# Kernel tuning notes

Hardware: AMD Instinct MI355X
Metric: run time of the kernel (lower is better)

## Reference

```python
import jax, jax.numpy as jnp
import numpy as np
from jax import lax

L_LAYERS = 8
HID = 300


def _reverse_padded(x, lengths):
    # x: [T, B, D]; reverse each sequence within its valid length, keep padding zero.
    T = x.shape[0]
    t = jnp.arange(T)[:, None]                      # [T,1]
    rev = lengths[None, :] - 1 - t                  # [T,B]
    valid = (rev >= 0)
    idx = jnp.clip(rev, 0, T - 1)
    g = jnp.take_along_axis(x, idx[:, :, None].astype(jnp.int32), axis=0)
    return g * valid[:, :, None].astype(x.dtype)


def _run_layer(x, W_ih, W_hh, b, lengths, reverse):
    # x: [T,B,D] time-major. W_ih: [D,6H], W_hh: [H,5H], b: [5H]
    T, B, _ = x.shape
    H = W_hh.shape[0]
    if reverse:
        x = _reverse_padded(x, lengths)
    pi = jnp.einsum('tbd,dg->tbg', x, W_ih)         # [T,B,6H] input projections
    mask = (jnp.arange(T)[:, None] < lengths[None, :])[:, :, None]  # [T,B,1] bool

    def step(carry, xt):
        h, c = carry
        pi_t, m = xt
        ps = h @ W_hh + b                            # [B,5H]
        z = pi_t[:, :5 * H] + ps                     # fused pre-activations
        i = jax.nn.sigmoid(z[:, 0 * H:1 * H])
        f = jax.nn.sigmoid(z[:, 1 * H:2 * H])
        g = jnp.tanh(z[:, 2 * H:3 * H])
        o = jax.nn.sigmoid(z[:, 3 * H:4 * H])
        r = jax.nn.sigmoid(z[:, 4 * H:5 * H])        # highway gate
        c_new = i * g + f * c
        lstm_out = o * jnp.tanh(c_new)
        h_new = r * lstm_out + (1.0 - r) * pi_t[:, 5 * H:]  # highway connection
        c = jnp.where(m, c_new, c)
        h = jnp.where(m, h_new, h)
        return (h, c), h_new * m.astype(h_new.dtype)

    init = (jnp.zeros((B, H), x.dtype), jnp.zeros((B, H), x.dtype))
    (_, _), ys = lax.scan(step, init, (pi, mask))
    if reverse:
        ys = _reverse_padded(ys, lengths)
    return ys


def setup_inputs() -> dict:
    key = jax.random.key(0)
    ks = jax.random.split(key, 6)
    B, T, D = 64, 256, 200
    inputs = jax.random.normal(ks[0], (B, T, D), dtype=jnp.float32)
    lengths = jnp.sort(jax.random.randint(ks[1], (B,), 1, T + 1))[::-1].astype(jnp.int32)
    s = 0.08
    W_ih0 = jax.random.normal(ks[2], (D, 6 * HID), dtype=jnp.float32) * s
    W_ih_rest = jax.random.normal(ks[3], (L_LAYERS - 1, HID, 6 * HID), dtype=jnp.float32) * s
    W_hh = jax.random.normal(ks[4], (L_LAYERS, HID, 5 * HID), dtype=jnp.float32) * s
    b_hh = jnp.zeros((L_LAYERS, 5 * HID), dtype=jnp.float32)
    b_hh = b_hh.at[:, HID:2 * HID].set(1.0)  # forget-gate bias init to 1
    return {"inputs": inputs, "lengths": lengths, "W_ih0": W_ih0,
            "W_ih_rest": W_ih_rest, "W_hh": W_hh, "b_hh": b_hh}


def reference(inputs, lengths, W_ih0, W_ih_rest, W_hh, b_hh):
    # inputs: [B,T,D] batch-first -> time-major [T,B,D]
    x = jnp.transpose(inputs, (1, 0, 2))
    per_layer = []
    for layer in range(L_LAYERS):
        Wih = W_ih0 if layer == 0 else W_ih_rest[layer - 1]
        x = _run_layer(x, Wih, W_hh[layer], b_hh[layer], lengths, reverse=(layer % 2 == 1))
        per_layer.append(x)
    hidden = jnp.stack(per_layer)                    # [L,T,B,H] (matches hy[:,1:])
    output = jnp.transpose(x, (1, 0, 2))             # [B,T,H], zero past lengths
    return output, hidden
```

## Files before the change

kernel.cpp:

```cpp
#include <hip/hip_runtime.h>
#include <hip/hip_bf16.h>

#define B_ 64
#define T_ 256
#define D_ 200
#define H_ 300
#define L_ 8
#define M_ 16384
#define NG 1800
#define NZ 1500
#define KP 320
#define NBP 1920

typedef __attribute__((ext_vector_type(8))) short bf16x8;
typedef __attribute__((ext_vector_type(4))) float f32x4;
typedef __attribute__((ext_vector_type(4))) unsigned u32x4;
typedef unsigned long long ull;

__device__ __forceinline__ unsigned short f2bf(float f) {
  union { float f; unsigned u; } v; v.f = f;
  unsigned r = v.u + 0x7fffu + ((v.u >> 16) & 1u);
  return (unsigned short)(r >> 16);
}

__device__ __forceinline__ float sigf(float x) { return 1.f / (1.f + __expf(-x)); }
__device__ __forceinline__ float tanhf_(float x) {
  x = fminf(15.f, fmaxf(-15.f, x));
  float e = __expf(2.f * x);
  return (e - 1.f) / (e + 1.f);
}

#define BARRIER() asm volatile("s_waitcnt lgkmcnt(0)\n\ts_barrier" ::: "memory")

__device__ __forceinline__ u32x4 ld128_nt(const ull* p) {
  u32x4 v;
  asm volatile("global_load_dwordx4 %0, %1, off nt\n\ts_waitcnt vmcnt(0)"
               : "=v"(v) : "v"(p) : "memory");
  return v;
}
__device__ __forceinline__ u32x4 ld128_sys(const ull* p) {
  u32x4 v;
  asm volatile("global_load_dwordx4 %0, %1, off sc0 sc1\n\ts_waitcnt vmcnt(0)"
               : "=v"(v) : "v"(p) : "memory");
  return v;
}
__device__ __forceinline__ void st64_plain(ull* p, ull v) {
  asm volatile("global_store_dwordx2 %0, %1, off" :: "v"(p), "v"(v) : "memory");
}
__device__ __forceinline__ void st64_sys(ull* p, ull v) {
  asm volatile("global_store_dwordx2 %0, %1, off sc0 sc1" :: "v"(p), "v"(v) : "memory");
}

__device__ __forceinline__ void gl_lds16(const unsigned short* g, unsigned short* l) {
  __builtin_amdgcn_global_load_lds(
      (const __attribute__((address_space(1))) void*)g,
      (__attribute__((address_space(3))) void*)l, 16, 0, 0);
}

__global__ void k_transpose_w(const float* __restrict__ W0, const float* __restrict__ Wr,
                              unsigned short* __restrict__ WbT) {
  __shared__ unsigned short t_lds[64][65];
  const int n0 = blockIdx.x * 64;
  const int k0 = blockIdx.y * 64;
  const int l = blockIdx.z;
  const int Kl = (l == 0) ? D_ : H_;
  const float* W = (l == 0) ? W0 : (Wr + (size_t)(l - 1) * H_ * NG);
  unsigned short* out = WbT + (size_t)l * NBP * KP;
  const int tx = threadIdx.x & 63;
  const int ty = threadIdx.x >> 6;
  #pragma unroll
  for (int i = 0; i < 16; i++) {
    int k = k0 + ty * 16 + i;
    int n = n0 + tx;
    float v = (k < Kl && n < NG) ? W[(size_t)k * NG + n] : 0.f;
    t_lds[ty * 16 + i][tx] = f2bf(v);
  }
  __syncthreads();
  #pragma unroll
  for (int i = 0; i < 16; i++) {
    int n = n0 + ty * 16 + i;
    if (n < NG) out[(size_t)n * KP + k0 + tx] = t_lds[tx][ty * 16 + i];
  }
}

__global__ void k_transpose_in(const float* __restrict__ inp, unsigned short* __restrict__ xb) {
  int i = blockIdx.x * blockDim.x + threadIdx.x;
  if (i >= T_ * B_ * D_) return;
  int d = i % D_;
  int r = i / D_;
  int b = r % B_;
  int t = r / B_;
  xb[(size_t)r * KP + d] = f2bf(inp[((size_t)b * T_ + t) * D_ + d]);
}

__global__ void k_out(const float* __restrict__ hid7, float* __restrict__ outp) {
  int i = blockIdx.x * blockDim.x + threadIdx.x;
  if (i >= B_ * T_ * H_) return;
  int j = i % H_;
  int r = i / H_;
  int t = r % T_;
  int b = r / T_;
  outp[i] = hid7[((size_t)t * B_ + b) * H_ + j];
}

__global__ __launch_bounds__(256) void k_gemm(const unsigned short* __restrict__ A,
                                              const unsigned short* __restrict__ Bt,
                                              float* __restrict__ C, int nk) {
  __shared__ unsigned short As[128 * 32];
  __shared__ unsigned short Bs[128 * 32];
  const int bm = blockIdx.x, bn = blockIdx.y;
  const int tid = threadIdx.x;
  const int lane = tid & 63, wid = tid >> 6;
  const int wm = wid & 1, wn = wid >> 1;
  const int l16 = lane & 15, quad = lane >> 4;
  const int srow = lane >> 2;
  const int sswz = ((lane & 3) ^ (srow & 3)) << 3;
  const int sA = ((quad ^ (l16 & 3)) << 3);
  const size_t arow0 = (size_t)bm * 128;
  const size_t brow0 = (size_t)bn * 128;
  f32x4 acc[4][4] = {};
  for (int kc = 0; kc < nk; kc++) {
    const int k0 = kc << 5;
    #pragma unroll
    for (int r = 0; r < 2; r++) {
      const int rbase = r * 64 + wid * 16;
      gl_lds16(A  + (arow0 + rbase + srow) * KP + k0 + sswz, &As[rbase * 32]);
      gl_lds16(Bt + (brow0 + rbase + srow) * KP + k0 + sswz, &Bs[rbase * 32]);
    }
    asm volatile("s_waitcnt vmcnt(0)" ::: "memory");
    __syncthreads();
    bf16x8 af[4], bfr[4];
    #pragma unroll
    for (int i = 0; i < 4; i++) {
      af[i]  = *(const bf16x8*)&As[(wm * 64 + i * 16 + l16) * 32 + sA];
      bfr[i] = *(const bf16x8*)&Bs[(wn * 64 + i * 16 + l16) * 32 + sA];
    }
    #pragma unroll
    for (int mi = 0; mi < 4; mi++)
      #pragma unroll
      for (int ni = 0; ni < 4; ni++)
        acc[mi][ni] = __builtin_amdgcn_mfma_f32_16x16x32_bf16(af[mi], bfr[ni], acc[mi][ni], 0, 0, 0);
    __syncthreads();
  }
  const int row0 = bm * 128 + wm * 64 + quad * 4;
  const int col0 = bn * 128 + wn * 64 + l16;
  #pragma unroll
  for (int mi = 0; mi < 4; mi++) {
    #pragma unroll
    for (int ni = 0; ni < 4; ni++) {
      int col = col0 + ni * 16;
      if (col < NG) {
        #pragma unroll
        for (int i = 0; i < 4; i++)
          C[(size_t)(row0 + mi * 16 + i) * NG + col] = acc[mi][ni][i];
      }
    }
  }
}

__global__ __launch_bounds__(512, 2) void k_recur(
    const float* __restrict__ pi, const float* __restrict__ Whh,
    const float* __restrict__ bias, const int* __restrict__ lens,
    float* __restrict__ hid, unsigned short* __restrict__ xb,
    ull* __restrict__ h_words, int rev, int tagbase)
{
  __shared__ __align__(16) unsigned short h_lds[16 * 328];
  __shared__ __align__(16) float z_lds[128 * 4];
  __shared__ float bias_s[128];
  __shared__ int len_s[4];

  const int tid = threadIdx.x;
  const int bid = blockIdx.x;
  const int g = bid & 15;
  const int cb = bid >> 4;

  const int lane = tid & 63;
  const int wid = tid >> 6;
  const int l16 = lane & 15;
  const int quad = lane >> 4;

  const int rp = tid / 25;
  const int gj = tid - rp * 25;
  const int j2 = cb * 25 + gj;

  bf16x8 wfrag[10];
  {
    int n = wid * 16 + l16;
    bool vn = n < 125;
    int colw = vn ? ((n / 25) * 300 + cb * 25 + (n % 25)) : 0;
    #pragma unroll
    for (int c = 0; c < 10; c++) {
      bf16x8 f;
      #pragma unroll
      for (int j = 0; j < 8; j++) {
        int k = c * 32 + quad * 8 + j;
        float v = (vn && k < 300) ? Whh[(size_t)k * NZ + colw] : 0.f;
        f[j] = (short)f2bf(v);
      }
      wfrag[c] = f;
    }
  }
  if (tid < 4) len_s[tid] = lens[g * 4 + tid];
  if (tid < 125) bias_s[tid] = bias[(tid / 25) * 300 + cb * 25 + (tid % 25)];
  for (int i = tid; i < 16 * 328; i += 512) h_lds[i] = 0;
  __syncthreads();

  int S = len_s[0];
  S = len_s[1] > S ? len_s[1] : S;
  S = len_s[2] > S ? len_s[2] : S;
  S = len_s[3] > S ? len_s[3] : S;

  ull* hwf = h_words + (size_t)g * 1200;
  ull* hws = h_words + 16 * 1200 + (size_t)g * 1200;
  const int brbase = g * 4;
  float cA = 0.f, cB = 0.f;

  float pA0 = 0.f, pA1 = 0.f, pA2 = 0.f, pA3 = 0.f, pA4 = 0.f, pA6 = 0.f;
  float pB0 = 0.f, pB1 = 0.f, pB2 = 0.f, pB3 = 0.f, pB4 = 0.f, pB6 = 0.f;
#define PI_PREF(ss) do {                                                          \
    int lrA_ = len_s[2 * rp], lrB_ = len_s[2 * rp + 1];                           \
    pA0 = pA1 = pA2 = pA3 = pA4 = pA6 = 0.f;                                      \
    pB0 = pB1 = pB2 = pB3 = pB4 = pB6 = 0.f;                                      \
    if ((ss) < lrA_) {                                                            \
      int t_ = rev ? (lrA_ - 1 - (ss)) : (ss);                                    \
      const float* pr_ = pi + ((size_t)t_ * B_ + (brbase + 2 * rp)) * NG;         \
      pA0 = pr_[j2]; pA1 = pr_[300 + j2]; pA2 = pr_[600 + j2];                    \
      pA3 = pr_[900 + j2]; pA4 = pr_[1200 + j2]; pA6 = pr_[NZ + j2];              \
    }                                                                             \
    if ((ss) < lrB_) {                                                            \
      int t_ = rev ? (lrB_ - 1 - (ss)) : (ss);                                    \
      const float* pr_ = pi + ((size_t)t_ * B_ + (brbase + 2 * rp + 1)) * NG;     \
      pB0 = pr_[j2]; pB1 = pr_[300 + j2]; pB2 = pr_[600 + j2];                    \
      pB3 = pr_[900 + j2]; pB4 = pr_[1200 + j2]; pB6 = pr_[NZ + j2];              \
    }                                                                             \
  } while (0)
  if (tid < 50) PI_PREF(0);

  for (int s = 0; s < S; s++) {
    if (s > 0 && tid >= 64 && tid < 364) {
      const unsigned tg = (unsigned)(tagbase + s);
      const size_t par = (size_t)(s & 1) * 600;
      const int pt = tid - 64;
      const ull* pf = hwf + par + 2 * pt;
      const ull* ps = hws + par + 2 * pt;
      u32x4 v;
      int miss = 0;
      for (;;) {
        v = ld128_nt(pf);
        if ((v.y == tg) && (v.w == tg)) break;
        if ((++miss & 31) == 0) {
          v = ld128_sys(ps);
          if ((v.y == tg) && (v.w == tg)) break;
          __builtin_amdgcn_s_sleep(1);
        }
      }
      int w0 = pt << 1;
      int r2 = (w0 >= 300) ? 1 : 0;
      int k = w0 - r2 * 300;
      h_lds[(2 * r2) * 328 + k]     = (unsigned short)(v.x >> 16);
      h_lds[(2 * r2 + 1) * 328 + k] = (unsigned short)(v.x & 0xffffu);
      int w1 = w0 + 1;
      int r2b = (w1 >= 300) ? 1 : 0;
      int kb = w1 - r2b * 300;
      h_lds[(2 * r2b) * 328 + kb]     = (unsigned short)(v.z >> 16);
      h_lds[(2 * r2b + 1) * 328 + kb] = (unsigned short)(v.z & 0xffffu);
    }
    BARRIER();

    f32x4 acc = {0, 0, 0, 0};
    if (s > 0) {
      f32x4 acc2 = {0, 0, 0, 0};
      const unsigned short* abase = &h_lds[l16 * 328 + quad * 8];
      #pragma unroll
      for (int c = 0; c < 10; c += 2) {
        bf16x8 a0 = *(const bf16x8*)(abase + c * 32);
        bf16x8 a1 = *(const bf16x8*)(abase + c * 32 + 32);
        acc  = __builtin_amdgcn_mfma_f32_16x16x32_bf16(a0, wfrag[c],     acc,  0, 0, 0);
        acc2 = __builtin_amdgcn_mfma_f32_16x16x32_bf16(a1, wfrag[c + 1], acc2, 0, 0, 0);
      }
      acc += acc2;
    }
    if (quad == 0) {
      int n = wid * 16 + l16;
      *(f32x4*)&z_lds[n * 4] = acc;
    }
    BARRIER();

    if (tid < 50) {
      const float bb0 = bias_s[gj],      bb1 = bias_s[25 + gj], bb2 = bias_s[50 + gj];
      const float bb3 = bias_s[75 + gj], bb4 = bias_s[100 + gj];
      const float2 z0 = *(const float2*)&z_lds[(gj      ) * 4 + 2 * rp];
      const float2 z1 = *(const float2*)&z_lds[(25 + gj ) * 4 + 2 * rp];
      const float2 z2 = *(const float2*)&z_lds[(50 + gj ) * 4 + 2 * rp];
      const float2 z3 = *(const float2*)&z_lds[(75 + gj ) * 4 + 2 * rp];
      const float2 z4 = *(const float2*)&z_lds[(100 + gj) * 4 + 2 * rp];
      float iA = sigf(z0.x + pA0 + bb0);
      float fA = sigf(z1.x + pA1 + bb1);
      float gA = tanhf_(z2.x + pA2 + bb2);
      float oA = sigf(z3.x + pA3 + bb3);
      float rA = sigf(z4.x + pA4 + bb4);
      float cnA = iA * gA + fA * cA; cA = cnA;
      float hA = rA * (oA * tanhf_(cnA)) + (1.f - rA) * pA6;
      float iB = sigf(z0.y + pB0 + bb0);
      float fB = sigf(z1.y + pB1 + bb1);
      float gB = tanhf_(z2.y + pB2 + bb2);
      float oB = sigf(z3.y + pB3 + bb3);
      float rB = sigf(z4.y + pB4 + bb4);
      float cnB = iB * gB + fB * cB; cB = cnB;
      float hB = rB * (oB * tanhf_(cnB)) + (1.f - rB) * pB6;

      unsigned short hbA = f2bf(hA), hbB = f2bf(hB);
      ull word = ((ull)(unsigned)(tagbase + s + 1) << 32)
               | ((unsigned)hbA << 16) | (unsigned)hbB;
      int pidx = ((s + 1) & 1) * 600 + rp * 300 + j2;
      st64_plain(hwf + pidx, word);
      st64_sys(hws + pidx, word);
      int lrA = len_s[2 * rp], lrB = len_s[2 * rp + 1];
      if (s < lrA) {
        int t = rev ? (lrA - 1 - s) : s;
        int br = brbase + 2 * rp;
        hid[((size_t)t * B_ + br) * H_ + j2] = hA;
        xb[((size_t)t * B_ + br) * KP + j2] = hbA;
      }
      if (s < lrB) {
        int t = rev ? (lrB - 1 - s) : s;
        int br = brbase + 2 * rp + 1;
        hid[((size_t)t * B_ + br) * H_ + j2] = hB;
        xb[((size_t)t * B_ + br) * KP + j2] = hbB;
      }
      PI_PREF(s + 1);
    }
  }
#undef PI_PREF
}

extern "C" void kernel_launch(void* const* d_in, const int* in_sizes, int n_in,
                              void* d_out, int out_size, void* d_ws, size_t ws_size,
                              hipStream_t stream) {
  const float* inputs = (const float*)d_in[0];
  const int* lengths = (const int*)d_in[1];
  const float* W_ih0 = (const float*)d_in[2];
  const float* W_ih_rest = (const float*)d_in[3];
  const float* W_hh = (const float*)d_in[4];
  const float* b_hh = (const float*)d_in[5];
  float* outp = (float*)d_out;
  float* hidden = outp + (size_t)B_ * T_ * H_;

  char* ws = (char*)d_ws;
  float* pi = (float*)ws;
  size_t off = (size_t)M_ * NG * 4;
  unsigned short* xb = (unsigned short*)(ws + off);
  off += (size_t)M_ * KP * 2;
  unsigned short* WbT = (unsigned short*)(ws + off);
  off += (size_t)L_ * NBP * KP * 2;
  ull* h_words = (ull*)(ws + off);
  size_t hw_bytes = 32ull * 1200 * 8;
  off += hw_bytes;

  hipMemsetAsync(d_out, 0, (size_t)out_size * 4, stream);
  hipMemsetAsync(h_words, 0, hw_bytes, stream);
  hipMemsetAsync(xb, 0, (size_t)M_ * KP * 2, stream);
  hipMemsetAsync(WbT, 0, (size_t)L_ * NBP * KP * 2, stream);

  k_transpose_w<<<dim3(29, 5, 8), 256, 0, stream>>>(W_ih0, W_ih_rest, WbT);
  {
    int n = T_ * B_ * D_;
    k_transpose_in<<<(n + 255) / 256, 256, 0, stream>>>(inputs, xb);
  }
  for (int l = 0; l < L_; l++) {
    const unsigned short* Bt = WbT + (size_t)l * NBP * KP;
    int nk = (l == 0) ? 7 : 10;
    k_gemm<<<dim3(M_ / 128, NBP / 128), 256, 0, stream>>>(xb, Bt, pi, nk);
    float* hid_l = hidden + (size_t)l * T_ * B_ * H_;
    k_recur<<<192, 512, 0, stream>>>(pi, W_hh + (size_t)l * H_ * NZ, b_hh + (size_t)l * NZ,
                                     lengths, hid_l, xb, h_words, l & 1, l * 300);
  }
  k_out<<<((B_ * T_ * H_) + 255) / 256, 256, 0, stream>>>(
      hidden + (size_t)(L_ - 1) * T_ * B_ * H_, outp);
}
```

Measured before the change: 3.473 ms.

## Interleave two batch groups per recurrent block to overlap polling with gate math

Each recurrent block now handles two independent batch groups, halving the grid from 192 to 96 blocks. The two groups run ping-pong, so one group's gate computation and stores overlap with polling for the other group's hidden state. Within each timestep the two groups' MFMA phases alternate. This is meant to hide the cross-block synchronization latency on the serial critical path. In exchange it adds shared-memory buffers and barriers per step and halves the number of active CUs.

```diff
diff --git a/kernel.cpp b/kernel.cpp
--- a/kernel.cpp
+++ b/kernel.cpp
@@ -158,21 +158,129 @@
   }
 }
 
+struct PiR { float v0, v1, v2, v3, v4, v6; };
+
+__device__ __forceinline__ void pi_pref_row(PiR& r, const float* __restrict__ pi,
+                                            int lr, int rev, int ss, int br, int j2) {
+  r.v0 = r.v1 = r.v2 = r.v3 = r.v4 = r.v6 = 0.f;
+  if (ss < lr) {
+    int t = rev ? (lr - 1 - ss) : ss;
+    const float* pr = pi + ((size_t)t * B_ + br) * NG;
+    r.v0 = pr[j2]; r.v1 = pr[300 + j2]; r.v2 = pr[600 + j2];
+    r.v3 = pr[900 + j2]; r.v4 = pr[1200 + j2]; r.v6 = pr[NZ + j2];
+  }
+}
+
+__device__ __forceinline__ void gates_grp(
+    float& c0, float& c1, PiR& pa, PiR& pb, int lA, int lB,
+    const float* z, const float* bias_s,
+    int rp, int gj, int j2, int brbase, int rev, int ss, int tagbase,
+    ull* hwf, ull* hws, float* hid, unsigned short* xb, const float* pi)
+{
+  const float bb0 = bias_s[gj],      bb1 = bias_s[25 + gj], bb2 = bias_s[50 + gj];
+  const float bb3 = bias_s[75 + gj], bb4 = bias_s[100 + gj];
+  const float2 z0 = *(const float2*)&z[(gj      ) * 4 + 2 * rp];
+  const float2 z1 = *(const float2*)&z[(25 + gj ) * 4 + 2 * rp];
+  const float2 z2 = *(const float2*)&z[(50 + gj ) * 4 + 2 * rp];
+  const float2 z3 = *(const float2*)&z[(75 + gj ) * 4 + 2 * rp];
+  const float2 z4 = *(const float2*)&z[(100 + gj) * 4 + 2 * rp];
+  float iA = sigf(z0.x + pa.v0 + bb0);
+  float fA = sigf(z1.x + pa.v1 + bb1);
+  float gA = tanhf_(z2.x + pa.v2 + bb2);
+  float oA = sigf(z3.x + pa.v3 + bb3);
+  float rA = sigf(z4.x + pa.v4 + bb4);
+  float cnA = iA * gA + fA * c0; c0 = cnA;
+  float hA = rA * (oA * tanhf_(cnA)) + (1.f - rA) * pa.v6;
+  float iB = sigf(z0.y + pb.v0 + bb0);
+  float fB = sigf(z1.y + pb.v1 + bb1);
+  float gB = tanhf_(z2.y + pb.v2 + bb2);
+  float oB = sigf(z3.y + pb.v3 + bb3);
+  float rB = sigf(z4.y + pb.v4 + bb4);
+  float cnB = iB * gB + fB * c1; c1 = cnB;
+  float hB = rB * (oB * tanhf_(cnB)) + (1.f - rB) * pb.v6;
+
+  unsigned short hbA = f2bf(hA), hbB = f2bf(hB);
+  ull word = ((ull)(unsigned)(tagbase + ss + 1) << 32)
+           | ((unsigned)hbA << 16) | (unsigned)hbB;
+  int pidx = ((ss + 1) & 1) * 600 + rp * 300 + j2;
+  st64_plain(hwf + pidx, word);
+  st64_sys(hws + pidx, word);
+  if (ss < lA) {
+    int t = rev ? (lA - 1 - ss) : ss;
+    int br = brbase + 2 * rp;
+    hid[((size_t)t * B_ + br) * H_ + j2] = hA;
+    xb[((size_t)t * B_ + br) * KP + j2] = hbA;
+  }
+  if (ss < lB) {
+    int t = rev ? (lB - 1 - ss) : ss;
+    int br = brbase + 2 * rp + 1;
+    hid[((size_t)t * B_ + br) * H_ + j2] = hB;
+    xb[((size_t)t * B_ + br) * KP + j2] = hbB;
+  }
+  pi_pref_row(pa, pi, lA, rev, ss + 1, brbase + 2 * rp, j2);
+  pi_pref_row(pb, pi, lB, rev, ss + 1, brbase + 2 * rp + 1, j2);
+}
+
+__device__ __forceinline__ void poll_stash(unsigned tg, int par, int pt,
+                                           const ull* hwf, const ull* hws,
+                                           unsigned short* h_lds) {
+  const ull* pf = hwf + par + 2 * pt;
+  const ull* ps = hws + par + 2 * pt;
+  u32x4 v;
+  int miss = 0;
+  for (;;) {
+    v = ld128_nt(pf);
+    if ((v.y == tg) && (v.w == tg)) break;
+    if ((++miss & 31) == 0) {
+      v = ld128_sys(ps);
+      if ((v.y == tg) && (v.w == tg)) break;
+      __builtin_amdgcn_s_sleep(1);
+    }
+  }
+  int w0 = pt << 1;
+  int r2 = (w0 >= 300) ? 1 : 0;
+  int k = w0 - r2 * 300;
+  h_lds[(2 * r2) * 328 + k]     = (unsigned short)(v.x >> 16);
+  h_lds[(2 * r2 + 1) * 328 + k] = (unsigned short)(v.x & 0xffffu);
+  int w1 = w0 + 1;
+  int r2b = (w1 >= 300) ? 1 : 0;
+  int kb = w1 - r2b * 300;
+  h_lds[(2 * r2b) * 328 + kb]     = (unsigned short)(v.z >> 16);
+  h_lds[(2 * r2b + 1) * 328 + kb] = (unsigned short)(v.z & 0xffffu);
+}
+
+__device__ __forceinline__ void mfma_phase(const unsigned short* h_lds, float* z_lds,
+                                           const bf16x8* wfrag, int l16, int quad, int wid) {
+  f32x4 acc = {0, 0, 0, 0}, acc2 = {0, 0, 0, 0};
+  const unsigned short* abase = &h_lds[l16 * 328 + quad * 8];
+  #pragma unroll
+  for (int c = 0; c < 10; c += 2) {
+    bf16x8 a0 = *(const bf16x8*)(abase + c * 32);
+    bf16x8 a1 = *(const bf16x8*)(abase + c * 32 + 32);
+    acc  = __builtin_amdgcn_mfma_f32_16x16x32_bf16(a0, wfrag[c],     acc,  0, 0, 0);
+    acc2 = __builtin_amdgcn_mfma_f32_16x16x32_bf16(a1, wfrag[c + 1], acc2, 0, 0, 0);
+  }
+  acc += acc2;
+  if (quad == 0) *(f32x4*)&z_lds[(wid * 16 + l16) * 4] = acc;
+}
+
 __global__ __launch_bounds__(512, 2) void k_recur(
     const float* __restrict__ pi, const float* __restrict__ Whh,
     const float* __restrict__ bias, const int* __restrict__ lens,
     float* __restrict__ hid, unsigned short* __restrict__ xb,
     ull* __restrict__ h_words, int rev, int tagbase)
 {
-  __shared__ __align__(16) unsigned short h_lds[16 * 328];
-  __shared__ __align__(16) float z_lds[128 * 4];
+  __shared__ __align__(16) unsigned short h_ldsA[16 * 328];
+  __shared__ __align__(16) unsigned short h_ldsB[16 * 328];
+  __shared__ __align__(16) float z_ldsA[128 * 4];
+  __shared__ __align__(16) float z_ldsB[128 * 4];
   __shared__ float bias_s[128];
-  __shared__ int len_s[4];
+  __shared__ int len_s8[8];
 
   const int tid = threadIdx.x;
   const int bid = blockIdx.x;
-  const int g = bid & 15;
-  const int cb = bid >> 4;
+  const int pairid = bid & 7;
+  const int cb = bid >> 3;
 
   const int lane = tid & 63;
   const int wid = tid >> 6;
@@ -200,138 +308,57 @@
       wfrag[c] = f;
     }
   }
-  if (tid < 4) len_s[tid] = lens[g * 4 + tid];
+  if (tid < 8) len_s8[tid] = lens[pairid * 8 + tid];
   if (tid < 125) bias_s[tid] = bias[(tid / 25) * 300 + cb * 25 + (tid % 25)];
-  for (int i = tid; i < 16 * 328; i += 512) h_lds[i] = 0;
+  for (int i = tid; i < 16 * 328; i += 512) { h_ldsA[i] = 0; h_ldsB[i] = 0; }
   __syncthreads();
 
-  int S = len_s[0];
-  S = len_s[1] > S ? len_s[1] : S;
-  S = len_s[2] > S ? len_s[2] : S;
-  S = len_s[3] > S ? len_s[3] : S;
-
-  ull* hwf = h_words + (size_t)g * 1200;
-  ull* hws = h_words + 16 * 1200 + (size_t)g * 1200;
-  const int brbase = g * 4;
-  float cA = 0.f, cB = 0.f;
-
-  float pA0 = 0.f, pA1 = 0.f, pA2 = 0.f, pA3 = 0.f, pA4 = 0.f, pA6 = 0.f;
-  float pB0 = 0.f, pB1 = 0.f, pB2 = 0.f, pB3 = 0.f, pB4 = 0.f, pB6 = 0.f;
-#define PI_PREF(ss) do {                                                          \
-    int lrA_ = len_s[2 * rp], lrB_ = len_s[2 * rp + 1];                           \
-    pA0 = pA1 = pA2 = pA3 = pA4 = pA6 = 0.f;                                      \
-    pB0 = pB1 = pB2 = pB3 = pB4 = pB6 = 0.f;                                      \
-    if ((ss) < lrA_) {                                                            \
-      int t_ = rev ? (lrA_ - 1 - (ss)) : (ss);                                    \
-      const float* pr_ = pi + ((size_t)t_ * B_ + (brbase + 2 * rp)) * NG;         \
-      pA0 = pr_[j2]; pA1 = pr_[300 + j2]; pA2 = pr_[600 + j2];                    \
-      pA3 = pr_[900 + j2]; pA4 = pr_[1200 + j2]; pA6 = pr_[NZ + j2];              \
-    }                                                                             \
-    if ((ss) < lrB_) {                                                            \
-      int t_ = rev ? (lrB_ - 1 - (ss)) : (ss);                                    \
-      const float* pr_ = pi + ((size_t)t_ * B_ + (brbase + 2 * rp + 1)) * NG;     \
-      pB0 = pr_[j2]; pB1 = pr_[300 + j2]; pB2 = pr_[600 + j2];                    \
-      pB3 = pr_[900 + j2]; pB4 = pr_[1200 + j2]; pB6 = pr_[NZ + j2];              \
-    }                                                                             \
-  } while (0)
-  if (tid < 50) PI_PREF(0);
+  int S = len_s8[0];
+  #pragma unroll
+  for (int i = 1; i < 8; i++) S = len_s8[i] > S ? len_s8[i] : S;
+
+  const int gA = 2 * pairid, gB = gA + 1;
+  ull* hwfA = h_words + (size_t)gA * 1200;
+  ull* hwsA = h_words + 16 * 1200 + (size_t)gA * 1200;
+  ull* hwfB = h_words + (size_t)gB * 1200;
+  ull* hwsB = h_words + 16 * 1200 + (size_t)gB * 1200;
+  const int brA = pairid * 8, brB = pairid * 8 + 4;
+
+  float cA0 = 0.f, cA1 = 0.f, cB0 = 0.f, cB1 = 0.f;
+  PiR pa, pb, pe, pf_;
+  int lA0 = 0, lA1 = 0, lB0 = 0, lB1 = 0;
+  if (tid < 50) {
+    lA0 = len_s8[2 * rp];     lA1 = len_s8[2 * rp + 1];
+    lB0 = len_s8[4 + 2 * rp]; lB1 = len_s8[4 + 2 * rp + 1];
+    pi_pref_row(pa,  pi, lA0, rev, 0, brA + 2 * rp,     j2);
+    pi_pref_row(pb,  pi, lA1, rev, 0, brA + 2 * rp + 1, j2);
+    pi_pref_row(pe,  pi, lB0, rev, 0, brB + 2 * rp,     j2);
+    pi_pref_row(pf_, pi, lB1, rev, 0, brB + 2 * rp + 1, j2);
+  }
 
   for (int s = 0; s < S; s++) {
-    if (s > 0 && tid >= 64 && tid < 364) {
-      const unsigned tg = (unsigned)(tagbase + s);
-      const size_t par = (size_t)(s & 1) * 600;
-      const int pt = tid - 64;
-      const ull* pf = hwf + par + 2 * pt;
-      const ull* ps = hws + par + 2 * pt;
-      u32x4 v;
-      int miss = 0;
-      for (;;) {
-        v = ld128_nt(pf);
-        if ((v.y == tg) && (v.w == tg)) break;
-        if ((++miss & 31) == 0) {
-          v = ld128_sys(ps);
-          if ((v.y == tg) && (v.w == tg)) break;
-          __builtin_amdgcn_s_sleep(1);
-        }
-      }
-      int w0 = pt << 1;
-      int r2 = (w0 >= 300) ? 1 : 0;
-      int k = w0 - r2 * 300;
-      h_lds[(2 * r2) * 328 + k]     = (unsigned short)(v.x >> 16);
-      h_lds[(2 * r2 + 1) * 328 + k] = (unsigned short)(v.x & 0xffffu);
-      int w1 = w0 + 1;
-      int r2b = (w1 >= 300) ? 1 : 0;
-      int kb = w1 - r2b * 300;
-      h_lds[(2 * r2b) * 328 + kb]     = (unsigned short)(v.z >> 16);
-      h_lds[(2 * r2b + 1) * 328 + kb] = (unsigned short)(v.z & 0xffffu);
+    if (s > 0) {
+      if (tid < 50)
+        gates_grp(cB0, cB1, pe, pf_, lB0, lB1, z_ldsB, bias_s,
+                  rp, gj, j2, brB, rev, s - 1, tagbase, hwfB, hwsB, hid, xb, pi);
+      else if (tid >= 64 && tid < 364)
+        poll_stash((unsigned)(tagbase + s), (s & 1) * 600, tid - 64, hwfA, hwsA, h_ldsA);
     }
     BARRIER();
-
-    f32x4 acc = {0, 0, 0, 0};
-    if (s > 0) {
-      f32x4 acc2 = {0, 0, 0, 0};
-      const unsigned short* abase = &h_lds[l16 * 328 + quad * 8];
-      #pragma unroll
-      for (int c = 0; c < 10; c += 2) {
-        bf16x8 a0 = *(const bf16x8*)(abase + c * 32);
-        bf16x8 a1 = *(const bf16x8*)(abase + c * 32 + 32);
-        acc  = __builtin_amdgcn_mfma_f32_16x16x32_bf16(a0, wfrag[c],     acc,  0, 0, 0);
-        acc2 = __builtin_amdgcn_mfma_f32_16x16x32_bf16(a1, wfrag[c + 1], acc2, 0, 0, 0);
-      }
-      acc += acc2;
-    }
-    if (quad == 0) {
-      int n = wid * 16 + l16;
-      *(f32x4*)&z_lds[n * 4] = acc;
-    }
+    mfma_phase(h_ldsA, z_ldsA, wfrag, l16, quad, wid);
     BARRIER();
-
-    if (tid < 50) {
-      const float bb0 = bias_s[gj],      bb1 = bias_s[25 + gj], bb2 = bias_s[50 + gj];
-      const float bb3 = bias_s[75 + gj], bb4 = bias_s[100 + gj];
-      const float2 z0 = *(const float2*)&z_lds[(gj      ) * 4 + 2 * rp];
-      const float2 z1 = *(const float2*)&z_lds[(25 + gj ) * 4 + 2 * rp];
-      const float2 z2 = *(const float2*)&z_lds[(50 + gj ) * 4 + 2 * rp];
-      const float2 z3 = *(const float2*)&z_lds[(75 + gj ) * 4 + 2 * rp];
-      const float2 z4 = *(const float2*)&z_lds[(100 + gj) * 4 + 2 * rp];
-      float iA = sigf(z0.x + pA0 + bb0);
-      float fA = sigf(z1.x + pA1 + bb1);
-      float gA = tanhf_(z2.x + pA2 + bb2);
-      float oA = sigf(z3.x + pA3 + bb3);
-      float rA = sigf(z4.x + pA4 + bb4);
-      float cnA = iA * gA + fA * cA; cA = cnA;
-      float hA = rA * (oA * tanhf_(cnA)) + (1.f - rA) * pA6;
-      float iB = sigf(z0.y + pB0 + bb0);
-      float fB = sigf(z1.y + pB1 + bb1);
-      float gB = tanhf_(z2.y + pB2 + bb2);
-      float oB = sigf(z3.y + pB3 + bb3);
-      float rB = sigf(z4.y + pB4 + bb4);
-      float cnB = iB * gB + fB * cB; cB = cnB;
-      float hB = rB * (oB * tanhf_(cnB)) + (1.f - rB) * pB6;
-
-      unsigned short hbA = f2bf(hA), hbB = f2bf(hB);
-      ull word = ((ull)(unsigned)(tagbase + s + 1) << 32)
-               | ((unsigned)hbA << 16) | (unsigned)hbB;
-      int pidx = ((s + 1) & 1) * 600 + rp * 300 + j2;
-      st64_plain(hwf + pidx, word);
-      st64_sys(hws + pidx, word);
-      int lrA = len_s[2 * rp], lrB = len_s[2 * rp + 1];
-      if (s < lrA) {
-        int t = rev ? (lrA - 1 - s) : s;
-        int br = brbase + 2 * rp;
-        hid[((size_t)t * B_ + br) * H_ + j2] = hA;
-        xb[((size_t)t * B_ + br) * KP + j2] = hbA;
-      }
-      if (s < lrB) {
-        int t = rev ? (lrB - 1 - s) : s;
-        int br = brbase + 2 * rp + 1;
-        hid[((size_t)t * B_ + br) * H_ + j2] = hB;
-        xb[((size_t)t * B_ + br) * KP + j2] = hbB;
-      }
-      PI_PREF(s + 1);
-    }
-  }
-#undef PI_PREF
+    if (tid < 50)
+      gates_grp(cA0, cA1, pa, pb, lA0, lA1, z_ldsA, bias_s,
+                rp, gj, j2, brA, rev, s, tagbase, hwfA, hwsA, hid, xb, pi);
+    else if (s > 0 && tid >= 64 && tid < 364)
+      poll_stash((unsigned)(tagbase + s), (s & 1) * 600, tid - 64, hwfB, hwsB, h_ldsB);
+    BARRIER();
+    mfma_phase(h_ldsB, z_ldsB, wfrag, l16, quad, wid);
+    BARRIER();
+  }
+  if (tid < 50)
+    gates_grp(cB0, cB1, pe, pf_, lB0, lB1, z_ldsB, bias_s,
+              rp, gj, j2, brB, rev, S - 1, tagbase, hwfB, hwsB, hid, xb, pi);
 }
 
 extern "C" void kernel_launch(void* const* d_in, const int* in_sizes, int n_in,
@@ -372,8 +399,8 @@
     int nk = (l == 0) ? 7 : 10;
     k_gemm<<<dim3(M_ / 128, NBP / 128), 256, 0, stream>>>(xb, Bt, pi, nk);
     float* hid_l = hidden + (size_t)l * T_ * B_ * H_;
-    k_recur<<<192, 512, 0, stream>>>(pi, W_hh + (size_t)l * H_ * NZ, b_hh + (size_t)l * NZ,
-                                     lengths, hid_l, xb, h_words, l & 1, l * 300);
+    k_recur<<<96, 512, 0, stream>>>(pi, W_hh + (size_t)l * H_ * NZ, b_hh + (size_t)l * NZ,
+                                    lengths, hid_l, xb, h_words, l & 1, l * 300);
   }
   k_out<<<((B_ * T_ * H_) + 255) / 256, 256, 0, stream>>>(
       hidden + (size_t)(L_ - 1) * T_ * B_ * H_, outp);
```

New measurement: 4.969 ms. +43.0%, slower.

## Widen recurrent blocks to 75 hidden units each, cutting grid to 64 blocks

Applied to the files above, without the earlier changes.

Each recurrence block now owns 75 hidden columns (375 gate outputs) instead of 25, with every wave holding three MFMA weight tiles in registers and 150 threads doing the elementwise cell update. The grid drops from 192 to 64 persistent blocks per layer. Fewer blocks take part in the per-step cross-block h exchange through global tagged words, which is meant to shorten the step barrier. In exchange each block does more MFMA and elementwise work per step, and holding 30 weight fragments per thread raises register pressure.

```diff
diff --git a/kernel.cpp b/kernel.cpp
--- a/kernel.cpp
+++ b/kernel.cpp
@@ -11,6 +11,10 @@
 #define NZ 1500
 #define KP 320
 #define NBP 1920
+#define JC 75
+#define ZC 375
+#define ZCP 384
+#define NT 3
 
 typedef __attribute__((ext_vector_type(8))) short bf16x8;
 typedef __attribute__((ext_vector_type(4))) float f32x4;
@@ -158,6 +162,47 @@
   }
 }
 
+struct PiR { float v0, v1, v2, v3, v4, v6; };
+
+__device__ __forceinline__ void pi_pref_row(PiR& r, const float* __restrict__ pi,
+                                            int lr, int rev, int ss, int br, int j2) {
+  r.v0 = r.v1 = r.v2 = r.v3 = r.v4 = r.v6 = 0.f;
+  if (ss < lr) {
+    int t = rev ? (lr - 1 - ss) : ss;
+    const float* pr = pi + ((size_t)t * B_ + br) * NG;
+    r.v0 = pr[j2]; r.v1 = pr[300 + j2]; r.v2 = pr[600 + j2];
+    r.v3 = pr[900 + j2]; r.v4 = pr[1200 + j2]; r.v6 = pr[NZ + j2];
+  }
+}
+
+__device__ __forceinline__ void poll_stash(unsigned tg, int par, int pt,
+                                           const ull* hwf, const ull* hws,
+                                           unsigned short* h_lds) {
+  const ull* pf = hwf + par + 2 * pt;
+  const ull* ps = hws + par + 2 * pt;
+  u32x4 v;
+  int miss = 0;
+  for (;;) {
+    v = ld128_nt(pf);
+    if ((v.y == tg) && (v.w == tg)) break;
+    if ((++miss & 31) == 0) {
+      v = ld128_sys(ps);
+      if ((v.y == tg) && (v.w == tg)) break;
+      __builtin_amdgcn_s_sleep(1);
+    }
+  }
+  int w0 = pt << 1;
+  int r2 = (w0 >= 300) ? 1 : 0;
+  int k = w0 - r2 * 300;
+  h_lds[(2 * r2) * 328 + k]     = (unsigned short)(v.x >> 16);
+  h_lds[(2 * r2 + 1) * 328 + k] = (unsigned short)(v.x & 0xffffu);
+  int w1 = w0 + 1;
+  int r2b = (w1 >= 300) ? 1 : 0;
+  int kb = w1 - r2b * 300;
+  h_lds[(2 * r2b) * 328 + kb]     = (unsigned short)(v.z >> 16);
+  h_lds[(2 * r2b + 1) * 328 + kb] = (unsigned short)(v.z & 0xffffu);
+}
+
 __global__ __launch_bounds__(512, 2) void k_recur(
     const float* __restrict__ pi, const float* __restrict__ Whh,
     const float* __restrict__ bias, const int* __restrict__ lens,
@@ -165,8 +210,8 @@
     ull* __restrict__ h_words, int rev, int tagbase)
 {
   __shared__ __align__(16) unsigned short h_lds[16 * 328];
-  __shared__ __align__(16) float z_lds[128 * 4];
-  __shared__ float bias_s[128];
+  __shared__ __align__(16) float z_lds[ZCP * 4];
+  __shared__ float bias_s[ZC];
   __shared__ int len_s[4];
 
   const int tid = threadIdx.x;
@@ -179,15 +224,16 @@
   const int l16 = lane & 15;
   const int quad = lane >> 4;
 
-  const int rp = tid / 25;
-  const int gj = tid - rp * 25;
-  const int j2 = cb * 25 + gj;
-
-  bf16x8 wfrag[10];
-  {
-    int n = wid * 16 + l16;
-    bool vn = n < 125;
-    int colw = vn ? ((n / 25) * 300 + cb * 25 + (n % 25)) : 0;
+  const int rp = tid / JC;
+  const int gj = tid - rp * JC;
+  const int j2 = cb * JC + gj;
+
+  bf16x8 wfrag[NT][10];
+  #pragma unroll
+  for (int ti = 0; ti < NT; ti++) {
+    int n = (wid * NT + ti) * 16 + l16;
+    bool vn = n < ZC;
+    int colw = vn ? ((n / JC) * 300 + cb * JC + (n % JC)) : 0;
     #pragma unroll
     for (int c = 0; c < 10; c++) {
       bf16x8 f;
@@ -197,11 +243,11 @@
         float v = (vn && k < 300) ? Whh[(size_t)k * NZ + colw] : 0.f;
         f[j] = (short)f2bf(v);
       }
-      wfrag[c] = f;
+      wfrag[ti][c] = f;
     }
   }
   if (tid < 4) len_s[tid] = lens[g * 4 + tid];
-  if (tid < 125) bias_s[tid] = bias[(tid / 25) * 300 + cb * 25 + (tid % 25)];
+  if (tid < ZC) bias_s[tid] = bias[(tid / JC) * 300 + cb * JC + (tid % JC)];
   for (int i = tid; i < 16 * 328; i += 512) h_lds[i] = 0;
   __syncthreads();
 
@@ -215,99 +261,62 @@
   const int brbase = g * 4;
   float cA = 0.f, cB = 0.f;
 
-  float pA0 = 0.f, pA1 = 0.f, pA2 = 0.f, pA3 = 0.f, pA4 = 0.f, pA6 = 0.f;
-  float pB0 = 0.f, pB1 = 0.f, pB2 = 0.f, pB3 = 0.f, pB4 = 0.f, pB6 = 0.f;
-#define PI_PREF(ss) do {                                                          \
-    int lrA_ = len_s[2 * rp], lrB_ = len_s[2 * rp + 1];                           \
-    pA0 = pA1 = pA2 = pA3 = pA4 = pA6 = 0.f;                                      \
-    pB0 = pB1 = pB2 = pB3 = pB4 = pB6 = 0.f;                                      \
-    if ((ss) < lrA_) {                                                            \
-      int t_ = rev ? (lrA_ - 1 - (ss)) : (ss);                                    \
-      const float* pr_ = pi + ((size_t)t_ * B_ + (brbase + 2 * rp)) * NG;         \
-      pA0 = pr_[j2]; pA1 = pr_[300 + j2]; pA2 = pr_[600 + j2];                    \
-      pA3 = pr_[900 + j2]; pA4 = pr_[1200 + j2]; pA6 = pr_[NZ + j2];              \
-    }                                                                             \
-    if ((ss) < lrB_) {                                                            \
-      int t_ = rev ? (lrB_ - 1 - (ss)) : (ss);                                    \
-      const float* pr_ = pi + ((size_t)t_ * B_ + (brbase + 2 * rp + 1)) * NG;     \
-      pB0 = pr_[j2]; pB1 = pr_[300 + j2]; pB2 = pr_[600 + j2];                    \
-      pB3 = pr_[900 + j2]; pB4 = pr_[1200 + j2]; pB6 = pr_[NZ + j2];              \
-    }                                                                             \
-  } while (0)
-  if (tid < 50) PI_PREF(0);
+  PiR pa, pb;
+  int lA = 0, lB = 0;
+  if (tid < 150) {
+    lA = len_s[2 * rp]; lB = len_s[2 * rp + 1];
+    pi_pref_row(pa, pi, lA, rev, 0, brbase + 2 * rp,     j2);
+    pi_pref_row(pb, pi, lB, rev, 0, brbase + 2 * rp + 1, j2);
+  }
 
   for (int s = 0; s < S; s++) {
-    if (s > 0 && tid >= 64 && tid < 364) {
-      const unsigned tg = (unsigned)(tagbase + s);
-      const size_t par = (size_t)(s & 1) * 600;
-      const int pt = tid - 64;
-      const ull* pf = hwf + par + 2 * pt;
-      const ull* ps = hws + par + 2 * pt;
-      u32x4 v;
-      int miss = 0;
-      for (;;) {
-        v = ld128_nt(pf);
-        if ((v.y == tg) && (v.w == tg)) break;
-        if ((++miss & 31) == 0) {
-          v = ld128_sys(ps);
-          if ((v.y == tg) && (v.w == tg)) break;
-          __builtin_amdgcn_s_sleep(1);
-        }
-      }
-      int w0 = pt << 1;
-      int r2 = (w0 >= 300) ? 1 : 0;
-      int k = w0 - r2 * 300;
-      h_lds[(2 * r2) * 328 + k]     = (unsigned short)(v.x >> 16);
-      h_lds[(2 * r2 + 1) * 328 + k] = (unsigned short)(v.x & 0xffffu);
-      int w1 = w0 + 1;
-      int r2b = (w1 >= 300) ? 1 : 0;
-      int kb = w1 - r2b * 300;
-      h_lds[(2 * r2b) * 328 + kb]     = (unsigned short)(v.z >> 16);
-      h_lds[(2 * r2b + 1) * 328 + kb] = (unsigned short)(v.z & 0xffffu);
-    }
+    if (s > 0 && tid >= 192 && tid < 492)
+      poll_stash((unsigned)(tagbase + s), (s & 1) * 600, tid - 192, hwf, hws, h_lds);
     BARRIER();
 
-    f32x4 acc = {0, 0, 0, 0};
-    if (s > 0) {
-      f32x4 acc2 = {0, 0, 0, 0};
+    {
+      f32x4 acc[NT] = {};
       const unsigned short* abase = &h_lds[l16 * 328 + quad * 8];
       #pragma unroll
-      for (int c = 0; c < 10; c += 2) {
-        bf16x8 a0 = *(const bf16x8*)(abase + c * 32);
-        bf16x8 a1 = *(const bf16x8*)(abase + c * 32 + 32);
-        acc  = __builtin_amdgcn_mfma_f32_16x16x32_bf16(a0, wfrag[c],     acc,  0, 0, 0);
-        acc2 = __builtin_amdgcn_mfma_f32_16x16x32_bf16(a1, wfrag[c + 1], acc2, 0, 0, 0);
-      }
-      acc += acc2;
-    }
-    if (quad == 0) {
-      int n = wid * 16 + l16;
-      *(f32x4*)&z_lds[n * 4] = acc;
+      for (int c = 0; c < 10; c++) {
+        bf16x8 a = *(const bf16x8*)(abase + c * 32);
+        #pragma unroll
+        for (int ti = 0; ti < NT; ti++)
+          acc[ti] = __builtin_amdgcn_mfma_f32_16x16x32_bf16(a, wfrag[ti][c], acc[ti], 0, 0, 0);
+      }
+      if (quad == 0) {
+        #pragma unroll
+        for (int ti = 0; ti < NT; ti++)
+          *(f32x4*)&z_lds[((wid * NT + ti) * 16 + l16) * 4] = acc[ti];
+      }
     }
     BARRIER();
 
-    if (tid < 50) {
-      const float bb0 = bias_s[gj],      bb1 = bias_s[25 + gj], bb2 = bias_s[50 + gj];
-      const float bb3 = bias_s[75 + gj], bb4 = bias_s[100 + gj];
-      const float2 z0 = *(const float2*)&z_lds[(gj      ) * 4 + 2 * rp];
-      const float2 z1 = *(const float2*)&z_lds[(25 + gj ) * 4 + 2 * rp];
-      const float2 z2 = *(const float2*)&z_lds[(50 + gj ) * 4 + 2 * rp];
-      const float2 z3 = *(const float2*)&z_lds[(75 + gj ) * 4 + 2 * rp];
-      const float2 z4 = *(const float2*)&z_lds[(100 + gj) * 4 + 2 * rp];
-      float iA = sigf(z0.x + pA0 + bb0);
-      float fA = sigf(z1.x + pA1 + bb1);
-      float gA = tanhf_(z2.x + pA2 + bb2);
-      float oA = sigf(z3.x + pA3 + bb3);
-      float rA = sigf(z4.x + pA4 + bb4);
+    if (tid < 150) {
+      const float bb0 = bias_s[gj];
+      const float bb1 = bias_s[JC + gj];
+      const float bb2 = bias_s[2 * JC + gj];
+      const float bb3 = bias_s[3 * JC + gj];
+      const float bb4 = bias_s[4 * JC + gj];
+      const float2 z0 = *(const float2*)&z_lds[(gj           ) * 4 + 2 * rp];
+      const float2 z1 = *(const float2*)&z_lds[(JC     + gj  ) * 4 + 2 * rp];
+      const float2 z2 = *(const float2*)&z_lds[(2 * JC + gj  ) * 4 + 2 * rp];
+      const float2 z3 = *(const float2*)&z_lds[(3 * JC + gj  ) * 4 + 2 * rp];
+      const float2 z4 = *(const float2*)&z_lds[(4 * JC + gj  ) * 4 + 2 * rp];
+      float iA = sigf(z0.x + pa.v0 + bb0);
+      float fA = sigf(z1.x + pa.v1 + bb1);
+      float gA = tanhf_(z2.x + pa.v2 + bb2);
+      float oA = sigf(z3.x + pa.v3 + bb3);
+      float rA = sigf(z4.x + pa.v4 + bb4);
       float cnA = iA * gA + fA * cA; cA = cnA;
-      float hA = rA * (oA * tanhf_(cnA)) + (1.f - rA) * pA6;
-      float iB = sigf(z0.y + pB0 + bb0);
-      float fB = sigf(z1.y + pB1 + bb1);
-      float gB = tanhf_(z2.y + pB2 + bb2);
-      float oB = sigf(z3.y + pB3 + bb3);
-      float rB = sigf(z4.y + pB4 + bb4);
+      float hA = rA * (oA * tanhf_(cnA)) + (1.f - rA) * pa.v6;
+      float iB = sigf(z0.y + pb.v0 + bb0);
+      float fB = sigf(z1.y + pb.v1 + bb1);
+      float gB = tanhf_(z2.y + pb.v2 + bb2);
+      float oB = sigf(z3.y + pb.v3 + bb3);
+      float rB = sigf(z4.y + pb.v4 + bb4);
       float cnB = iB * gB + fB * cB; cB = cnB;
-      float hB = rB * (oB * tanhf_(cnB)) + (1.f - rB) * pB6;
+      float hB = rB * (oB * tanhf_(cnB)) + (1.f - rB) * pb.v6;
 
       unsigned short hbA = f2bf(hA), hbB = f2bf(hB);
       ull word = ((ull)(unsigned)(tagbase + s + 1) << 32)
@@ -315,23 +324,22 @@
       int pidx = ((s + 1) & 1) * 600 + rp * 300 + j2;
       st64_plain(hwf + pidx, word);
       st64_sys(hws + pidx, word);
-      int lrA = len_s[2 * rp], lrB = len_s[2 * rp + 1];
-      if (s < lrA) {
-        int t = rev ? (lrA - 1 - s) : s;
+      if (s < lA) {
+        int t = rev ? (lA - 1 - s) : s;
         int br = brbase + 2 * rp;
         hid[((size_t)t * B_ + br) * H_ + j2] = hA;
         xb[((size_t)t * B_ + br) * KP + j2] = hbA;
       }
-      if (s < lrB) {
-        int t = rev ? (lrB - 1 - s) : s;
+      if (s < lB) {
+        int t = rev ? (lB - 1 - s) : s;
         int br = brbase + 2 * rp + 1;
         hid[((size_t)t * B_ + br) * H_ + j2] = hB;
         xb[((size_t)t * B_ + br) * KP + j2] = hbB;
       }
-      PI_PREF(s + 1);
-    }
-  }
-#undef PI_PREF
+      pi_pref_row(pa, pi, lA, rev, s + 1, brbase + 2 * rp,     j2);
+      pi_pref_row(pb, pi, lB, rev, s + 1, brbase + 2 * rp + 1, j2);
+    }
+  }
 }
 
 extern "C" void kernel_launch(void* const* d_in, const int* in_sizes, int n_in,
@@ -372,8 +380,8 @@
     int nk = (l == 0) ? 7 : 10;
     k_gemm<<<dim3(M_ / 128, NBP / 128), 256, 0, stream>>>(xb, Bt, pi, nk);
     float* hid_l = hidden + (size_t)l * T_ * B_ * H_;
-    k_recur<<<192, 512, 0, stream>>>(pi, W_hh + (size_t)l * H_ * NZ, b_hh + (size_t)l * NZ,
-                                     lengths, hid_l, xb, h_words, l & 1, l * 300);
+    k_recur<<<64, 512, 0, stream>>>(pi, W_hh + (size_t)l * H_ * NZ, b_hh + (size_t)l * NZ,
+                                    lengths, hid_l, xb, h_words, l & 1, l * 300);
   }
   k_out<<<((B_ * T_ * H_) + 255) / 256, 256, 0, stream>>>(
       hidden + (size_t)(L_ - 1) * T_ * B_ * H_, outp);
```

Measured after the change: 4.386 ms. +26.3%, slower.
